# Optimization experiments

Measured on AMD Instinct MI355X. Metric: run time of the kernel, lower is better.

## Reference

```python
import jax, jax.numpy as jnp
from jax import lax
import numpy as np

B, T, D, H, O, L = 64, 1024, 256, 512, 256, 2


def setup_inputs() -> dict:
    key = jax.random.key(0)
    ks = jax.random.split(key, 12)
    s_in = 1.0 / np.sqrt(H)
    inp = {
        "x": jax.random.normal(ks[0], (B, T, D), dtype=jnp.float32),
        "W_ih0": jax.random.uniform(ks[1], (H, D), jnp.float32, -s_in, s_in),
        "W_hh0": jax.random.uniform(ks[2], (H, H), jnp.float32, -s_in, s_in),
        "b_ih0": jax.random.uniform(ks[3], (H,), jnp.float32, -s_in, s_in),
        "b_hh0": jax.random.uniform(ks[4], (H,), jnp.float32, -s_in, s_in),
        "W_ih1": jax.random.uniform(ks[5], (H, H), jnp.float32, -s_in, s_in),
        "W_hh1": jax.random.uniform(ks[6], (H, H), jnp.float32, -s_in, s_in),
        "b_ih1": jax.random.uniform(ks[7], (H,), jnp.float32, -s_in, s_in),
        "b_hh1": jax.random.uniform(ks[8], (H,), jnp.float32, -s_in, s_in),
        "W_fc": jax.random.uniform(ks[9], (O, H), jnp.float32, -s_in, s_in),
        "b_fc": jax.random.uniform(ks[10], (O,), jnp.float32, -s_in, s_in),
    }
    return inp


def _rnn_layer(inp, W_ih, W_hh, b_ih, b_hh):
    # inp: [B, T, Din] -> outputs [B, T, H], final hidden [B, H]
    # PyTorch: h_t = tanh(x_t @ W_ih^T + b_ih + h_{t-1} @ W_hh^T + b_hh)
    xW = jnp.einsum("btd,hd->bth", inp, W_ih) + b_ih + b_hh  # precompute input proj

    def step(h, xw_t):
        h = jnp.tanh(xw_t + h @ W_hh.T)
        return h, h

    h0 = jnp.zeros((inp.shape[0], W_hh.shape[0]), dtype=inp.dtype)
    hT, hs = lax.scan(step, h0, jnp.swapaxes(xW, 0, 1))  # scan over time
    return jnp.swapaxes(hs, 0, 1), hT


def reference(x, W_ih0, W_hh0, b_ih0, b_hh0, W_ih1, W_hh1, b_ih1, b_hh1, W_fc, b_fc):
    out0, _ = _rnn_layer(x, W_ih0, W_hh0, b_ih0, b_hh0)
    _, hT1 = _rnn_layer(out0, W_ih1, W_hh1, b_ih1, b_hh1)
    # fc applied to hn[-1] (last layer final hidden state)
    return hT1 @ W_fc.T + b_fc  # [B, O]
```

## Files before the change

### kernel.cpp

```cpp
#include <hip/hip_runtime.h>
#include <cmath>


#define Bdim 64
#define Tdim 1024
#define Ddim 256
#define Hdim 512
#define Odim 256

template <int K>
__global__ __launch_bounds__(1024) void gemm_rows(const float* A, const float* W,
                                                  const float* __restrict__ bias_a,
                                                  const float* __restrict__ bias_b,
                                                  float* C) {
  constexpr int KT = 16;
  __shared__ __align__(16) float As[64][KT];
  __shared__ __align__(16) float Ws[KT][516];
  const int t = threadIdx.x;
  const size_t row0 = (size_t)blockIdx.x * 64;
  const int tn = t & 127;
  const int tm = t >> 7;

  float acc[8][4];
#pragma unroll
  for (int i = 0; i < 8; ++i)
#pragma unroll
    for (int j = 0; j < 4; ++j) acc[i][j] = 0.f;

  const int r_st = t >> 4;
  const int k_st = t & 15;

  for (int k0 = 0; k0 < K; k0 += KT) {
    As[r_st][k_st] = A[(row0 + r_st) * K + k0 + k_st];
#pragma unroll
    for (int rep = 0; rep < 8; ++rep) {
      const int idx = rep * 1024 + t;
      const int n = idx >> 4;
      const int kk = idx & 15;
      Ws[kk][n] = W[(size_t)n * K + k0 + kk];
    }
    __syncthreads();
#pragma unroll
    for (int kk = 0; kk < KT; ++kk) {
      float a[8];
#pragma unroll
      for (int i = 0; i < 8; ++i) a[i] = As[tm * 8 + i][kk];
      const float4 w = *(const float4*)&Ws[kk][tn * 4];
#pragma unroll
      for (int i = 0; i < 8; ++i) {
        acc[i][0] = fmaf(a[i], w.x, acc[i][0]);
        acc[i][1] = fmaf(a[i], w.y, acc[i][1]);
        acc[i][2] = fmaf(a[i], w.z, acc[i][2]);
        acc[i][3] = fmaf(a[i], w.w, acc[i][3]);
      }
    }
    __syncthreads();
  }
  float bn[4];
#pragma unroll
  for (int j = 0; j < 4; ++j) bn[j] = bias_a[tn * 4 + j] + bias_b[tn * 4 + j];
#pragma unroll
  for (int i = 0; i < 8; ++i) {
    float4 v;
    v.x = acc[i][0] + bn[0];
    v.y = acc[i][1] + bn[1];
    v.z = acc[i][2] + bn[2];
    v.w = acc[i][3] + bn[3];
    *(float4*)&C[(row0 + tm * 8 + i) * (size_t)Hdim + tn * 4] = v;
  }
}

__device__ __forceinline__ float fast_tanh(float y) {
  const float e2 = __expf(2.0f * y);
  return 1.0f - 2.0f * __builtin_amdgcn_rcpf(e2 + 1.0f);
}

__device__ __forceinline__ unsigned ld_l2_sc0(const unsigned* p) {
  unsigned v;
  asm volatile("global_load_dword %0, %1, off sc0\n\ts_waitcnt vmcnt(0)"
               : "=v"(v)
               : "v"(p)
               : "memory");
  return v;
}
__device__ __forceinline__ void st_l2_sc0(unsigned* p, unsigned v) {
  asm volatile("global_store_dword %0, %1, off sc0" ::"v"(p), "v"(v) : "memory");
}

__global__ __launch_bounds__(512, 2) void rnn_scan_coop(
    float* xw,
    const float* __restrict__ Whh,
    unsigned* hbuf,
    unsigned* fbuf,
    float* h_final,
    const int store_seq) {
  const int bi = blockIdx.x;
  const int b = bi & 63;
  const int q = bi >> 6;
  const int t = threadIdx.x;
  const int w = t >> 6;
  const int l = t & 63;
  const int jg0 = q * 128 + 2 * l;
  const bool is_epi = ((w >> 1) == q);

  __shared__ __align__(16) float hL[2][Hdim];
  __shared__ __align__(16) float red[2][8][128];

  float4 W0[16], W1[16];
  {
    const float4* w0p = (const float4*)(Whh + (size_t)jg0 * Hdim + w * 64);
    const float4* w1p = (const float4*)(Whh + (size_t)(jg0 + 1) * Hdim + w * 64);
#pragma unroll
    for (int c = 0; c < 16; ++c) {
      W0[c] = w0p[c];
      W1[c] = w1p[c];
    }
  }
#pragma unroll
  for (int c = 0; c < 16; ++c) {
    asm volatile("" : "+v"(W0[c].x), "+v"(W0[c].y), "+v"(W0[c].z), "+v"(W0[c].w));
    asm volatile("" : "+v"(W1[c].x), "+v"(W1[c].y), "+v"(W1[c].z), "+v"(W1[c].w));
  }

  hL[0][t] = 0.0f;
  __syncthreads();

  float* row = xw + (size_t)b * Tdim * Hdim;
  unsigned* hb_row = hbuf + b * Hdim;
  unsigned* fb_row = fbuf + b * Hdim;
  float xv = is_epi ? row[t] : 0.f;

  for (int s = 0; s < Tdim; ++s, row += Hdim) {
    const int sp = s & 1;

    if (s > 0 && !is_epi) {
      const size_t off = (size_t)((s - 1) & 1) * (Bdim * Hdim) + t;
      const unsigned want = 1024u | ((unsigned)s & 1023u);
      const unsigned* fp = fb_row + off;
      const unsigned* sp_ = hb_row + off;
      unsigned v = ld_l2_sc0(fp);
      if ((v & 2047u) != want) {
        for (;;) {
          v = ld_l2_sc0(fp);
          if ((v & 2047u) == want) break;
          v = ld_l2_sc0(fp);
          if ((v & 2047u) == want) break;
          v = __hip_atomic_load(sp_, __ATOMIC_RELAXED, __HIP_MEMORY_SCOPE_AGENT);
          if ((v & 2047u) == want) break;
        }
      }
      hL[sp][t] = __uint_as_float(v & 0xFFFFF800u);
    }

    const float4* h4 = (const float4*)&hL[sp][w * 64];
    float a0 = 0.f, a0b = 0.f, a1 = 0.f, a1b = 0.f;
#pragma unroll
    for (int c = 0; c < 16; ++c) {
      const float4 hv = h4[c];
      a0  = fmaf(W0[c].x, hv.x, a0);
      a0b = fmaf(W0[c].y, hv.y, a0b);
      a0  = fmaf(W0[c].z, hv.z, a0);
      a0b = fmaf(W0[c].w, hv.w, a0b);
      a1  = fmaf(W1[c].x, hv.x, a1);
      a1b = fmaf(W1[c].y, hv.y, a1b);
      a1  = fmaf(W1[c].z, hv.z, a1);
      a1b = fmaf(W1[c].w, hv.w, a1b);
    }
    *(float2*)&red[sp][w][2 * l] = make_float2(a0 + a0b, a1 + a1b);
    __syncthreads();

    if (is_epi) {
      const int e = t & 127;
      float y = xv;
#pragma unroll
      for (int w8 = 0; w8 < 8; ++w8) y += red[sp][w8][e];
      const float hn = fast_tanh(y);
      const unsigned bits = (__float_as_uint(hn) + 0x400u) & 0xFFFFF800u;
      const float hq = __uint_as_float(bits);
      const unsigned pv = bits | 1024u | ((unsigned)(s + 1) & 1023u);
      const size_t off = (size_t)sp * (Bdim * Hdim) + t;
      st_l2_sc0(fb_row + off, pv);
      __hip_atomic_store(hb_row + off, pv, __ATOMIC_RELAXED,
                         __HIP_MEMORY_SCOPE_AGENT);
      hL[sp ^ 1][t] = hq;
      if (store_seq) row[t] = hq;
      if (s + 1 < Tdim)
        xv = row[Hdim + t];
      else if (h_final != nullptr)
        h_final[(size_t)b * Hdim + t] = hq;
    }
  }
}

__global__ __launch_bounds__(256) void fc_kernel(const float* __restrict__ h,
                                                 const float* __restrict__ Wfc,
                                                 const float* __restrict__ bfc,
                                                 float* __restrict__ out) {
  __shared__ float hs[Hdim];
  const int b = blockIdx.x, o = threadIdx.x;
  hs[o] = h[(size_t)b * Hdim + o];
  hs[o + 256] = h[(size_t)b * Hdim + 256 + o];
  __syncthreads();
  float acc = bfc[o];
  const float* wr = Wfc + (size_t)o * Hdim;
#pragma unroll 4
  for (int k = 0; k < Hdim; k += 4) {
    const float4 w = *(const float4*)(wr + k);
    acc = fmaf(w.x, hs[k], acc);
    acc = fmaf(w.y, hs[k + 1], acc);
    acc = fmaf(w.z, hs[k + 2], acc);
    acc = fmaf(w.w, hs[k + 3], acc);
  }
  out[(size_t)b * Odim + o] = acc;
}

extern "C" void kernel_launch(void* const* d_in, const int* in_sizes, int n_in,
                              void* d_out, int out_size, void* d_ws, size_t ws_size,
                              hipStream_t stream) {
  const float* x = (const float*)d_in[0];
  const float* W_ih0 = (const float*)d_in[1];
  const float* W_hh0 = (const float*)d_in[2];
  const float* b_ih0 = (const float*)d_in[3];
  const float* b_hh0 = (const float*)d_in[4];
  const float* W_ih1 = (const float*)d_in[5];
  const float* W_hh1 = (const float*)d_in[6];
  const float* b_ih1 = (const float*)d_in[7];
  const float* b_hh1 = (const float*)d_in[8];
  const float* W_fc = (const float*)d_in[9];
  const float* b_fc = (const float*)d_in[10];
  float* out = (float*)d_out;

  float* A = (float*)d_ws;
  unsigned* hbuf0 = (unsigned*)(A + (size_t)Bdim * Tdim * Hdim);
  unsigned* hbuf1 = hbuf0 + (size_t)2 * Bdim * Hdim;
  unsigned* fbuf0 = hbuf1 + (size_t)2 * Bdim * Hdim;
  unsigned* fbuf1 = fbuf0 + (size_t)2 * Bdim * Hdim;
  float* hT1 = (float*)(fbuf1 + (size_t)2 * Bdim * Hdim);

  gemm_rows<Ddim><<<(Bdim * Tdim) / 64, 1024, 0, stream>>>(x, W_ih0, b_ih0, b_hh0, A);

  {
    float* xwp = A;
    const float* W = W_hh0;
    unsigned* hb = hbuf0;
    unsigned* fb = fbuf0;
    float* hf = nullptr;
    int ss = 1;
    void* args[] = {&xwp, (void*)&W, &hb, &fb, &hf, &ss};
    hipLaunchCooperativeKernel((void*)rnn_scan_coop, dim3(Bdim * 4), dim3(512),
                               args, 0, stream);
  }

  gemm_rows<Hdim><<<(Bdim * Tdim) / 64, 1024, 0, stream>>>(A, W_ih1, b_ih1, b_hh1, A);

  {
    float* xwp = A;
    const float* W = W_hh1;
    unsigned* hb = hbuf1;
    unsigned* fb = fbuf1;
    float* hf = hT1;
    int ss = 0;
    void* args[] = {&xwp, (void*)&W, &hb, &fb, &hf, &ss};
    hipLaunchCooperativeKernel((void*)rnn_scan_coop, dim3(Bdim * 4), dim3(512),
                               args, 0, stream);
  }

  fc_kernel<<<Bdim, Odim, 0, stream>>>(hT1, W_fc, b_fc, out);
}
```

Baseline: 3.282 ms.

## Interleave two batch rows per block in the recurrent scan to hide sync latency

```diff
diff --git a/kernel.cpp b/kernel.cpp
--- a/kernel.cpp
+++ b/kernel.cpp
@@ -87,7 +87,7 @@
   asm volatile("global_store_dword %0, %1, off sc0" ::"v"(p), "v"(v) : "memory");
 }
 
-__global__ __launch_bounds__(512, 2) void rnn_scan_coop(
+__global__ __launch_bounds__(512, 2) void rnn_scan2(
     float* xw,
     const float* __restrict__ Whh,
     unsigned* hbuf,
@@ -95,16 +95,20 @@
     float* h_final,
     const int store_seq) {
   const int bi = blockIdx.x;
-  const int b = bi & 63;
-  const int q = bi >> 6;
+  const int p = bi & 31;
+  const int q = bi >> 5;
+  const int rA = 2 * p;
+  const int rB = 2 * p + 1;
   const int t = threadIdx.x;
   const int w = t >> 6;
   const int l = t & 63;
   const int jg0 = q * 128 + 2 * l;
   const bool is_epi = ((w >> 1) == q);
 
-  __shared__ __align__(16) float hL[2][Hdim];
-  __shared__ __align__(16) float red[2][8][128];
+  __shared__ __align__(16) float hLA[2][Hdim];
+  __shared__ __align__(16) float hLB[2][Hdim];
+  __shared__ __align__(16) float redA[2][8][128];
+  __shared__ __align__(16) float redB[2][8][128];
 
   float4 W0[16], W1[16];
   {
@@ -122,22 +126,27 @@
     asm volatile("" : "+v"(W1[c].x), "+v"(W1[c].y), "+v"(W1[c].z), "+v"(W1[c].w));
   }
 
-  hL[0][t] = 0.0f;
+  hLA[0][t] = 0.0f;
+  hLB[0][t] = 0.0f;
   __syncthreads();
 
-  float* row = xw + (size_t)b * Tdim * Hdim;
-  unsigned* hb_row = hbuf + b * Hdim;
-  unsigned* fb_row = fbuf + b * Hdim;
-  float xv = is_epi ? row[t] : 0.f;
-
-  for (int s = 0; s < Tdim; ++s, row += Hdim) {
+  float* rowA = xw + (size_t)rA * Tdim * Hdim;
+  float* rowB = xw + (size_t)rB * Tdim * Hdim;
+  unsigned* hbA = hbuf + rA * Hdim;
+  unsigned* fbA = fbuf + rA * Hdim;
+  unsigned* hbB = hbuf + rB * Hdim;
+  unsigned* fbB = fbuf + rB * Hdim;
+  float xvA = is_epi ? rowA[t] : 0.f;
+  float xvB = is_epi ? rowB[t] : 0.f;
+
+  for (int s = 0; s < Tdim; ++s, rowA += Hdim, rowB += Hdim) {
     const int sp = s & 1;
+    const unsigned want = 1024u | ((unsigned)s & 1023u);
 
     if (s > 0 && !is_epi) {
       const size_t off = (size_t)((s - 1) & 1) * (Bdim * Hdim) + t;
-      const unsigned want = 1024u | ((unsigned)s & 1023u);
-      const unsigned* fp = fb_row + off;
-      const unsigned* sp_ = hb_row + off;
+      const unsigned* fp = fbA + off;
+      const unsigned* mp = hbA + off;
       unsigned v = ld_l2_sc0(fp);
       if ((v & 2047u) != want) {
         for (;;) {
@@ -145,49 +154,107 @@
           if ((v & 2047u) == want) break;
           v = ld_l2_sc0(fp);
           if ((v & 2047u) == want) break;
-          v = __hip_atomic_load(sp_, __ATOMIC_RELAXED, __HIP_MEMORY_SCOPE_AGENT);
+          v = __hip_atomic_load(mp, __ATOMIC_RELAXED, __HIP_MEMORY_SCOPE_AGENT);
           if ((v & 2047u) == want) break;
         }
       }
-      hL[sp][t] = __uint_as_float(v & 0xFFFFF800u);
-    }
-
-    const float4* h4 = (const float4*)&hL[sp][w * 64];
-    float a0 = 0.f, a0b = 0.f, a1 = 0.f, a1b = 0.f;
-#pragma unroll
-    for (int c = 0; c < 16; ++c) {
-      const float4 hv = h4[c];
-      a0  = fmaf(W0[c].x, hv.x, a0);
-      a0b = fmaf(W0[c].y, hv.y, a0b);
-      a0  = fmaf(W0[c].z, hv.z, a0);
-      a0b = fmaf(W0[c].w, hv.w, a0b);
-      a1  = fmaf(W1[c].x, hv.x, a1);
-      a1b = fmaf(W1[c].y, hv.y, a1b);
-      a1  = fmaf(W1[c].z, hv.z, a1);
-      a1b = fmaf(W1[c].w, hv.w, a1b);
-    }
-    *(float2*)&red[sp][w][2 * l] = make_float2(a0 + a0b, a1 + a1b);
+      hLA[sp][t] = __uint_as_float(v & 0xFFFFF800u);
+    }
+    {
+      const float4* h4 = (const float4*)&hLA[sp][w * 64];
+      float a0 = 0.f, a0b = 0.f, a1 = 0.f, a1b = 0.f;
+#pragma unroll
+      for (int c = 0; c < 16; ++c) {
+        const float4 hv = h4[c];
+        a0  = fmaf(W0[c].x, hv.x, a0);
+        a0b = fmaf(W0[c].y, hv.y, a0b);
+        a0  = fmaf(W0[c].z, hv.z, a0);
+        a0b = fmaf(W0[c].w, hv.w, a0b);
+        a1  = fmaf(W1[c].x, hv.x, a1);
+        a1b = fmaf(W1[c].y, hv.y, a1b);
+        a1  = fmaf(W1[c].z, hv.z, a1);
+        a1b = fmaf(W1[c].w, hv.w, a1b);
+      }
+      *(float2*)&redA[sp][w][2 * l] = make_float2(a0 + a0b, a1 + a1b);
+    }
     __syncthreads();
 
     if (is_epi) {
       const int e = t & 127;
-      float y = xv;
-#pragma unroll
-      for (int w8 = 0; w8 < 8; ++w8) y += red[sp][w8][e];
+      float y = xvA;
+#pragma unroll
+      for (int w8 = 0; w8 < 8; ++w8) y += redA[sp][w8][e];
       const float hn = fast_tanh(y);
       const unsigned bits = (__float_as_uint(hn) + 0x400u) & 0xFFFFF800u;
       const float hq = __uint_as_float(bits);
       const unsigned pv = bits | 1024u | ((unsigned)(s + 1) & 1023u);
       const size_t off = (size_t)sp * (Bdim * Hdim) + t;
-      st_l2_sc0(fb_row + off, pv);
-      __hip_atomic_store(hb_row + off, pv, __ATOMIC_RELAXED,
+      st_l2_sc0(fbA + off, pv);
+      __hip_atomic_store(hbA + off, pv, __ATOMIC_RELAXED,
                          __HIP_MEMORY_SCOPE_AGENT);
-      hL[sp ^ 1][t] = hq;
-      if (store_seq) row[t] = hq;
+      hLA[sp ^ 1][t] = hq;
+      if (store_seq) rowA[t] = hq;
       if (s + 1 < Tdim)
-        xv = row[Hdim + t];
+        xvA = rowA[Hdim + t];
       else if (h_final != nullptr)
-        h_final[(size_t)b * Hdim + t] = hq;
+        h_final[(size_t)rA * Hdim + t] = hq;
+    }
+
+    if (s > 0 && !is_epi) {
+      const size_t off = (size_t)((s - 1) & 1) * (Bdim * Hdim) + t;
+      const unsigned* fp = fbB + off;
+      const unsigned* mp = hbB + off;
+      unsigned v = ld_l2_sc0(fp);
+      if ((v & 2047u) != want) {
+        for (;;) {
+          v = ld_l2_sc0(fp);
+          if ((v & 2047u) == want) break;
+          v = ld_l2_sc0(fp);
+          if ((v & 2047u) == want) break;
+          v = __hip_atomic_load(mp, __ATOMIC_RELAXED, __HIP_MEMORY_SCOPE_AGENT);
+          if ((v & 2047u) == want) break;
+        }
+      }
+      hLB[sp][t] = __uint_as_float(v & 0xFFFFF800u);
+    }
+    {
+      const float4* h4 = (const float4*)&hLB[sp][w * 64];
+      float a0 = 0.f, a0b = 0.f, a1 = 0.f, a1b = 0.f;
+#pragma unroll
+      for (int c = 0; c < 16; ++c) {
+        const float4 hv = h4[c];
+        a0  = fmaf(W0[c].x, hv.x, a0);
+        a0b = fmaf(W0[c].y, hv.y, a0b);
+        a0  = fmaf(W0[c].z, hv.z, a0);
+        a0b = fmaf(W0[c].w, hv.w, a0b);
+        a1  = fmaf(W1[c].x, hv.x, a1);
+        a1b = fmaf(W1[c].y, hv.y, a1b);
+        a1  = fmaf(W1[c].z, hv.z, a1);
+        a1b = fmaf(W1[c].w, hv.w, a1b);
+      }
+      *(float2*)&redB[sp][w][2 * l] = make_float2(a0 + a0b, a1 + a1b);
+    }
+    __syncthreads();
+
+    if (is_epi) {
+      const int e = t & 127;
+      float y = xvB;
+#pragma unroll
+      for (int w8 = 0; w8 < 8; ++w8) y += redB[sp][w8][e];
+      const float hn = fast_tanh(y);
+      const unsigned bits = (__float_as_uint(hn) + 0x400u) & 0xFFFFF800u;
+      const float hq = __uint_as_float(bits);
+      const unsigned pv = bits | 1024u | ((unsigned)(s + 1) & 1023u);
+      const size_t off = (size_t)sp * (Bdim * Hdim) + t;
+      st_l2_sc0(fbB + off, pv);
+      __hip_atomic_store(hbB + off, pv, __ATOMIC_RELAXED,
+                         __HIP_MEMORY_SCOPE_AGENT);
+      hLB[sp ^ 1][t] = hq;
+      if (store_seq) rowB[t] = hq;
+      if (s + 1 < Tdim)
+        xvB = rowB[Hdim + t];
+      else if (h_final != nullptr)
+        h_final[(size_t)rB * Hdim + t] = hq;
     }
   }
 }
@@ -247,7 +314,7 @@
     float* hf = nullptr;
     int ss = 1;
     void* args[] = {&xwp, (void*)&W, &hb, &fb, &hf, &ss};
-    hipLaunchCooperativeKernel((void*)rnn_scan_coop, dim3(Bdim * 4), dim3(512),
+    hipLaunchCooperativeKernel((void*)rnn_scan2, dim3(Bdim * 2), dim3(512),
                                args, 0, stream);
   }
 
@@ -261,7 +328,7 @@
     float* hf = hT1;
     int ss = 0;
     void* args[] = {&xwp, (void*)&W, &hb, &fb, &hf, &ss};
-    hipLaunchCooperativeKernel((void*)rnn_scan_coop, dim3(Bdim * 4), dim3(512),
+    hipLaunchCooperativeKernel((void*)rnn_scan2, dim3(Bdim * 2), dim3(512),
                                args, 0, stream);
   }
 
```

After: 6.304 ms. +92.1%, slower.
